# Performance work log

Measured on AMD Instinct MI355X. Metric: run time of the kernel, lower is better.

## Reference

```python
import jax, jax.numpy as jnp
import numpy as np

EMB_DIM = 768
NUM_HEADS = 12
OUT_DIM = 768


def setup_inputs() -> dict:
    key = jax.random.key(0)
    k_x, k_q, k_k, k_v, k_o = jax.random.split(key, 5)
    B, N, D = 8, 1024, EMB_DIM
    s = 1.0 / np.sqrt(D)
    return {
        "x": jax.random.normal(k_x, (B, N, D), dtype=jnp.float32),
        # torch nn.Linear weights are stored [out_features, in_features]
        "Wq": jax.random.normal(k_q, (D, D), dtype=jnp.float32) * s,
        "Wk": jax.random.normal(k_k, (D, D), dtype=jnp.float32) * s,
        "Wv": jax.random.normal(k_v, (D, D), dtype=jnp.float32) * s,
        "Wo": jax.random.normal(k_o, (OUT_DIM, D), dtype=jnp.float32) * s,
    }


def _split_heads(t, H):
    # [B, N, D] -> [B*H, N, D//H]  (heads folded into batch, per einsum 'b i d')
    B, N, D = t.shape
    return t.reshape(B, N, H, D // H).transpose(0, 2, 1, 3).reshape(B * H, N, D // H)


def _merge_heads(t, B, H):
    BH, N, dh = t.shape
    return t.reshape(B, H, N, dh).transpose(0, 2, 1, 3).reshape(B, N, H * dh)


def reference(x, Wq, Wk, Wv, Wo):
    B, N, D = x.shape
    H = NUM_HEADS
    dh = D // H
    # q/k/v projections (torch Linear: y = x @ W.T, no bias)
    q = _split_heads(x @ Wq.T, H)
    k = _split_heads(x @ Wk.T, H)
    v = _split_heads(x @ Wv.T, H)
    scale = dh ** (-0.5)
    # dots: 'b i d , b j d -> b i j' -> full [B*H, N, N] score matrix
    dots = jnp.einsum('bid,bjd->bij', q, k) * scale
    attn = jax.nn.softmax(dots, axis=-1)
    # dropout p=0.0 -> identity
    # vect: 'b i d , b d j -> b i j' == attn @ v
    vect = jnp.einsum('bij,bjd->bid', attn, v)
    out = _merge_heads(vect, B, H) @ Wo.T
    return out
```

## Files before the change

### kernel.cpp

```cpp
#include <hip/hip_runtime.h>
#include <hip/hip_bf16.h>
#include <stdint.h>


typedef __bf16 bf16x8 __attribute__((ext_vector_type(8)));
typedef __bf16 bf16x4 __attribute__((ext_vector_type(4)));
typedef float f32x4 __attribute__((ext_vector_type(4)));

#define GAS __attribute__((address_space(1)))
#define LAS __attribute__((address_space(3)))

__device__ __forceinline__ void glds16(const short* gp, short* lp) {
  __builtin_amdgcn_global_load_lds((const GAS void*)gp, (LAS void*)lp, 16, 0, 0);
}

__device__ __forceinline__ float fast_exp2(float x) {
#if __has_builtin(__builtin_amdgcn_exp2f)
  return __builtin_amdgcn_exp2f(x);
#else
  return __expf(x * 0.6931471805599453f);
#endif
}

__device__ __forceinline__ short bfbits(float f) {
  __bf16 b = (__bf16)f;
  union { __bf16 b; short s; } cv; cv.b = b;
  return cv.s;
}

__device__ __forceinline__ void stage8_f32(const float* __restrict__ src, short* dst) {
  float4 f0 = ((const float4*)src)[0];
  float4 f1 = ((const float4*)src)[1];
  bf16x8 t;
  t[0] = (__bf16)f0.x; t[1] = (__bf16)f0.y; t[2] = (__bf16)f0.z; t[3] = (__bf16)f0.w;
  t[4] = (__bf16)f1.x; t[5] = (__bf16)f1.y; t[6] = (__bf16)f1.z; t[7] = (__bf16)f1.w;
  *(bf16x8*)dst = t;
}

__global__ __launch_bounds__(256) void convert_kernel(
    const float* __restrict__ x, const float* __restrict__ Wq,
    const float* __restrict__ Wk, const float* __restrict__ Wv,
    const float* __restrict__ Wo,
    short* __restrict__ xb, short* __restrict__ wqkv, short* __restrict__ wob) {
  int u0 = blockIdx.x * 1024 + threadIdx.x;
#pragma unroll
  for (int i = 0; i < 4; ++i) {
    int u = u0 + i * 256;
    const float* src; short* dst;
    if (u < 786432) { src = x + (size_t)u * 8; dst = xb + (size_t)u * 8; }
    else if (u < 1007616) {
      int r = u - 786432;
      int wsel = r / 73728, off = r % 73728;
      const float* W = (wsel == 0) ? Wq : (wsel == 1) ? Wk : Wv;
      src = W + (size_t)off * 8;
      dst = wqkv + (size_t)r * 8;
    } else {
      int r = u - 1007616;
      src = Wo + (size_t)r * 8; dst = wob + (size_t)r * 8;
    }
    stage8_f32(src, dst);
  }
}

__device__ __forceinline__ void stage_half(const short* __restrict__ g, short* l,
                                           int w, int lane) {
#pragma unroll
  for (int p = 0; p < 2; ++p) {
    int c = (w * 2 + p) * 64 + lane;
    int row = c >> 3;
    int cs = ((c & 7) ^ (row & 7)) * 8;
    glds16(g + (size_t)row * 768 + cs, l + c * 8);
  }
}

__device__ __forceinline__ void bar_fence() {
  asm volatile("" ::: "memory");
  __builtin_amdgcn_s_barrier();
  asm volatile("" ::: "memory");
}

__device__ __forceinline__ void load_a8(const short* base, int wr, int l16, int quad,
                                        bf16x8 (&fa)[4][2]) {
#pragma unroll
  for (int mf = 0; mf < 4; ++mf)
#pragma unroll
    for (int kk = 0; kk < 2; ++kk) {
      int row = wr * 64 + mf * 16 + l16;
      fa[mf][kk] = *(const bf16x8*)&base[row * 64 + ((((kk << 2) + quad) ^ (row & 7)) << 3)];
    }
}

__device__ __forceinline__ void load_b4(const short* base, int rbase, int l16, int quad,
                                        bf16x8 (&fb)[2][2]) {
#pragma unroll
  for (int nf = 0; nf < 2; ++nf)
#pragma unroll
    for (int kk = 0; kk < 2; ++kk) {
      int row = rbase + nf * 16 + l16;
      fb[nf][kk] = *(const bf16x8*)&base[row * 64 + ((((kk << 2) + quad) ^ (row & 7)) << 3)];
    }
}

__device__ __forceinline__ void mma16(const bf16x8 (&fa)[4][2], const bf16x8 (&fb)[2][2],
                                      f32x4 (&acc)[4][4], int nf0) {
  __builtin_amdgcn_s_setprio(1);
#pragma unroll
  for (int kk = 0; kk < 2; ++kk)
#pragma unroll
    for (int mf = 0; mf < 4; ++mf)
#pragma unroll
      for (int nf = 0; nf < 2; ++nf)
        acc[mf][nf0 + nf] = __builtin_amdgcn_mfma_f32_16x16x32_bf16(
            fa[mf][kk], fb[nf][kk], acc[mf][nf0 + nf], 0, 0, 0);
  __builtin_amdgcn_s_setprio(0);
}

__global__ __launch_bounds__(512, 2) void gemm_qkv(
    const short* __restrict__ xb, const short* __restrict__ wqkv,
    short* __restrict__ q, short* __restrict__ k, short* __restrict__ vt) {
  const int lin = blockIdx.x;
  const int xcd = lin & 7, grp = lin >> 3;
  const int by = grp >> 3;
  const int bx = xcd * 8 + (grp & 7);
  const int m0 = bx * 128;
  const int n0g = by * 256;
  const int tid = threadIdx.x;
  const int w = tid >> 6, lane = tid & 63, l16 = lane & 15, quad = lane >> 4;
  const int wr = w >> 2, wc = w & 3;

  __shared__ short lds[3][24576];

  const short* Asrc = xb + (size_t)m0 * 768;
  const short* Bsrc = wqkv + (size_t)n0g * 768;

  f32x4 acc[4][4];
#pragma unroll
  for (int i = 0; i < 4; ++i)
#pragma unroll
    for (int j = 0; j < 4; ++j) acc[i][j] = (f32x4){0.f, 0.f, 0.f, 0.f};

  stage_half(Asrc, &lds[0][0], w, lane);
  stage_half(Bsrc, &lds[0][8192], w, lane);
  stage_half(Bsrc + 98304, &lds[0][16384], w, lane);
  stage_half(Asrc + 64, &lds[1][0], w, lane);
  stage_half(Bsrc + 64, &lds[1][8192], w, lane);
  stage_half(Bsrc + 98304 + 64, &lds[1][16384], w, lane);
  asm volatile("s_waitcnt vmcnt(6)" ::: "memory");
  bar_fence();

  const int bh = wc >> 1;
  const int rb0 = (wc & 1) * 64;

  bf16x8 fa[4][2], fb0[2][2], fb1[2][2];

#pragma unroll
  for (int t = 0; t < 12; ++t) {
    const int buf = t % 3, nb = (t + 2) % 3;
    const bool pf = (t < 10);
    const short* A = &lds[buf][0];
    const short* Bb = &lds[buf][8192 + bh * 8192];

    load_a8(A, wr, l16, quad, fa);
    load_b4(Bb, rb0, l16, quad, fb0);
    if (pf) {
      stage_half(Asrc + (size_t)(t + 2) * 64, &lds[nb][0], w, lane);
      stage_half(Bsrc + (size_t)(t + 2) * 64, &lds[nb][8192], w, lane);
    }
    bar_fence();
    __builtin_amdgcn_sched_barrier(0);
    mma16(fa, fb0, acc, 0);
    __builtin_amdgcn_sched_barrier(0);
    bar_fence();

    load_b4(Bb, rb0 + 32, l16, quad, fb1);
    if (pf) {
      stage_half(Bsrc + 98304 + (size_t)(t + 2) * 64, &lds[nb][16384], w, lane);
      asm volatile("s_waitcnt vmcnt(6)" ::: "memory");
    } else if (t == 10) {
      asm volatile("s_waitcnt vmcnt(0)" ::: "memory");
    }
    bar_fence();
    __builtin_amdgcn_sched_barrier(0);
    mma16(fa, fb1, acc, 2);
    __builtin_amdgcn_sched_barrier(0);
    bar_fence();
  }

  const int wsel = by / 3;
  const int nl0 = (by % 3) * 256 + wc * 64;
  if (wsel == 2) {
#pragma unroll
    for (int mf = 0; mf < 4; ++mf)
#pragma unroll
      for (int nf = 0; nf < 4; ++nf) {
        int token = m0 + wr * 64 + mf * 16 + quad * 4;
        int nl = nl0 + nf * 16 + l16;
        int bhh = (token >> 10) * 12 + (nl >> 6);
        short tmp[4];
#pragma unroll
        for (int r = 0; r < 4; ++r) tmp[r] = bfbits(acc[mf][nf][r]);
        *(uint2*)(vt + (size_t)bhh * 65536 + (size_t)(nl & 63) * 1024 + (token & 1023)) =
            *(const uint2*)tmp;
      }
  } else {
    short* C = wsel ? k : q;
    const float sc = wsel ? 1.0f : 0.1803368801111244f;
#pragma unroll
    for (int mf = 0; mf < 4; ++mf)
#pragma unroll
      for (int nf = 0; nf < 4; ++nf)
#pragma unroll
        for (int r = 0; r < 4; ++r) {
          int row = m0 + wr * 64 + mf * 16 + quad * 4 + r;
          int nl = nl0 + nf * 16 + l16;
          C[(size_t)row * 768 + nl] = bfbits(acc[mf][nf][r] * sc);
        }
  }
}

__global__ __launch_bounds__(256, 3) void attn_kernel(
    const short* __restrict__ q, const short* __restrict__ k,
    const short* __restrict__ vt, short* __restrict__ vect) {
  const int bh = blockIdx.x % 96;
  const int qt = blockIdx.x / 96;
  const int b = bh / 12, h = bh % 12;
  const int m0 = qt * 128;
  const int tid = threadIdx.x;
  const int w = tid >> 6, lane = tid & 63, l16 = lane & 15, quad = lane >> 4;

  __shared__ short sK[128 * 64];
  __shared__ short sVt[64 * 128];

  const size_t base = (size_t)b * 786432 + (size_t)h * 64;
  const size_t vbase = (size_t)bh * 65536;

#pragma unroll
  for (int p = 0; p < 4; ++p) {
    int lin = (w * 4 + p) * 64 + lane;
    int row = lin >> 3;
    int cs = ((lin & 7) ^ (row & 7)) * 8;
    glds16(q + base + (size_t)(m0 + row) * 768 + cs, &sK[lin * 8]);
  }
  __syncthreads();
  bf16x8 bq[2][2];
#pragma unroll
  for (int g = 0; g < 2; ++g)
#pragma unroll
    for (int kk = 0; kk < 2; ++kk) {
      int row = g * 64 + w * 16 + l16;
      bq[g][kk] = *(const bf16x8*)&sK[row * 64 + (((kk * 4 + quad) ^ (row & 7)) << 3)];
    }

  f32x4 l4[2];
  l4[0] = (f32x4){0.f, 0.f, 0.f, 0.f};
  l4[1] = (f32x4){0.f, 0.f, 0.f, 0.f};
  f32x4 oacc[2][4];
#pragma unroll
  for (int g = 0; g < 2; ++g)
#pragma unroll
    for (int td = 0; td < 4; ++td) oacc[g][td] = (f32x4){0.f, 0.f, 0.f, 0.f};

  for (int j0 = 0; j0 < 1024; j0 += 128) {
    __syncthreads();
#pragma unroll
    for (int p = 0; p < 4; ++p) {
      int lin = (w * 4 + p) * 64 + lane;
      int row = lin >> 3;
      int cs = ((lin & 7) ^ (row & 7)) * 8;
      glds16(k + base + (size_t)(j0 + row) * 768 + cs, &sK[lin * 8]);
    }
#pragma unroll
    for (int p = 0; p < 4; ++p) {
      int lin = (w * 4 + p) * 64 + lane;
      int row = lin >> 4;
      int c = lin & 15;
      int cs = (c ^ (row & 15)) * 8;
      glds16(vt + vbase + (size_t)row * 1024 + j0 + cs, &sVt[lin * 8]);
    }
    __syncthreads();

#pragma unroll
    for (int jh = 0; jh < 2; ++jh) {
      f32x4 s[2][4];
#pragma unroll
      for (int g = 0; g < 2; ++g)
#pragma unroll
        for (int ti = 0; ti < 4; ++ti) s[g][ti] = (f32x4){0.f, 0.f, 0.f, 0.f};
#pragma unroll
      for (int kk = 0; kk < 2; ++kk)
#pragma unroll
        for (int ti = 0; ti < 4; ++ti) {
          int row = jh * 64 + ti * 16 + l16;
          bf16x8 a = *(const bf16x8*)&sK[row * 64 + (((kk * 4 + quad) ^ (row & 7)) << 3)];
          s[0][ti] = __builtin_amdgcn_mfma_f32_16x16x32_bf16(a, bq[0][kk], s[0][ti], 0, 0, 0);
          s[1][ti] = __builtin_amdgcn_mfma_f32_16x16x32_bf16(a, bq[1][kk], s[1][ti], 0, 0, 0);
        }

      bf16x4 pb[2][4];
#pragma unroll
      for (int g = 0; g < 2; ++g)
#pragma unroll
        for (int ti = 0; ti < 4; ++ti) {
          f32x4 e;
          e[0] = fast_exp2(s[g][ti][0]);
          e[1] = fast_exp2(s[g][ti][1]);
          e[2] = fast_exp2(s[g][ti][2]);
          e[3] = fast_exp2(s[g][ti][3]);
          l4[g] += e;
          bf16x4 tb;
          tb[0] = (__bf16)e[0]; tb[1] = (__bf16)e[1];
          tb[2] = (__bf16)e[2]; tb[3] = (__bf16)e[3];
          pb[g][ti] = tb;
        }

#pragma unroll
      for (int t2 = 0; t2 < 2; ++t2) {
        union { bf16x4 hh[2]; bf16x8 v; } bp0, bp1;
        bp0.hh[0] = pb[0][2 * t2];
        bp0.hh[1] = pb[0][2 * t2 + 1];
        bp1.hh[0] = pb[1][2 * t2];
        bp1.hh[1] = pb[1][2 * t2 + 1];
#pragma unroll
        for (int td = 0; td < 4; ++td) {
          int row = td * 16 + l16;
          int o1 = jh * 64 + t2 * 32 + quad * 4;
          int c1 = o1 >> 3, w1 = o1 & 7;
          int c2 = c1 + 2;
          union { uint2 u[2]; bf16x8 v; } tmp;
          tmp.u[0] = *(const uint2*)&sVt[row * 128 + ((c1 ^ (row & 15)) << 3) + w1];
          tmp.u[1] = *(const uint2*)&sVt[row * 128 + ((c2 ^ (row & 15)) << 3) + w1];
          oacc[0][td] = __builtin_amdgcn_mfma_f32_16x16x32_bf16(tmp.v, bp0.v, oacc[0][td], 0, 0, 0);
          oacc[1][td] = __builtin_amdgcn_mfma_f32_16x16x32_bf16(tmp.v, bp1.v, oacc[1][td], 0, 0, 0);
        }
      }
    }
  }

#pragma unroll
  for (int g = 0; g < 2; ++g) {
    float l = (l4[g][0] + l4[g][1]) + (l4[g][2] + l4[g][3]);
    l += __shfl_xor(l, 16);
    l += __shfl_xor(l, 32);
    float inv = 1.0f / l;
    int i_tok = m0 + g * 64 + w * 16 + l16;
#pragma unroll
    for (int td = 0; td < 4; ++td) {
      short tmp[4];
#pragma unroll
      for (int r = 0; r < 4; ++r) tmp[r] = bfbits(oacc[g][td][r] * inv);
      *(uint2*)(vect + base + (size_t)i_tok * 768 + td * 16 + quad * 4) = *(const uint2*)tmp;
    }
  }
}

__global__ __launch_bounds__(256) void gemm_out(
    const short* __restrict__ vect, const short* __restrict__ wob,
    float* __restrict__ out) {
  const int m0 = blockIdx.x * 64;
  const int n0 = blockIdx.y * 128;
  const int tid = threadIdx.x;
  const int w = tid >> 6, lane = tid & 63, l16 = lane & 15, quad = lane >> 4;
  const int wr = w >> 1, wc = w & 1;

  __shared__ short sA[64 * 64];
  __shared__ short sB[128 * 64];

  f32x4 acc[2][4];
#pragma unroll
  for (int i = 0; i < 2; ++i)
#pragma unroll
    for (int j = 0; j < 4; ++j) acc[i][j] = (f32x4){0.f, 0.f, 0.f, 0.f};

  for (int k0 = 0; k0 < 768; k0 += 64) {
    __syncthreads();
    const short* Ab = vect + (size_t)m0 * 768 + k0;
    const short* Bb = wob + (size_t)n0 * 768 + k0;
#pragma unroll
    for (int p = 0; p < 2; ++p) {
      int lin = (w * 2 + p) * 64 + lane;
      int row = lin >> 3;
      int cs = ((lin & 7) ^ (row & 7)) * 8;
      glds16(Ab + (size_t)row * 768 + cs, &sA[lin * 8]);
    }
#pragma unroll
    for (int p = 0; p < 4; ++p) {
      int lin = (w * 4 + p) * 64 + lane;
      int row = lin >> 3;
      int cs = ((lin & 7) ^ (row & 7)) * 8;
      glds16(Bb + (size_t)row * 768 + cs, &sB[lin * 8]);
    }
    __syncthreads();
#pragma unroll
    for (int kk2 = 0; kk2 < 2; ++kk2) {
      bf16x8 af[2], bfg[4];
#pragma unroll
      for (int t = 0; t < 2; ++t) {
        int ra = wr * 32 + t * 16 + l16;
        af[t] = *(const bf16x8*)&sA[ra * 64 + (((kk2 * 4 + quad) ^ (ra & 7)) << 3)];
      }
#pragma unroll
      for (int t = 0; t < 4; ++t) {
        int rb = wc * 64 + t * 16 + l16;
        bfg[t] = *(const bf16x8*)&sB[rb * 64 + (((kk2 * 4 + quad) ^ (rb & 7)) << 3)];
      }
#pragma unroll
      for (int ti = 0; ti < 2; ++ti)
#pragma unroll
        for (int tj = 0; tj < 4; ++tj)
          acc[ti][tj] = __builtin_amdgcn_mfma_f32_16x16x32_bf16(af[ti], bfg[tj], acc[ti][tj], 0, 0, 0);
    }
  }
#pragma unroll
  for (int ti = 0; ti < 2; ++ti)
#pragma unroll
    for (int tj = 0; tj < 4; ++tj)
#pragma unroll
      for (int r = 0; r < 4; ++r) {
        int row = m0 + wr * 32 + ti * 16 + quad * 4 + r;
        int col = n0 + wc * 64 + tj * 16 + l16;
        out[(size_t)row * 768 + col] = acc[ti][tj][r];
      }
}

extern "C" void kernel_launch(void* const* d_in, const int* in_sizes, int n_in,
                              void* d_out, int out_size, void* d_ws, size_t ws_size,
                              hipStream_t stream) {
  const float* x  = (const float*)d_in[0];
  const float* Wq = (const float*)d_in[1];
  const float* Wk = (const float*)d_in[2];
  const float* Wv = (const float*)d_in[3];
  const float* Wo = (const float*)d_in[4];
  float* out = (float*)d_out;

  const size_t MN = (size_t)8192 * 768;
  short* q    = (short*)d_ws;
  short* k    = q + MN;
  short* vt   = k + MN;
  short* vect = q;
  short* wob  = vt + MN;

  short* xb   = (short*)d_out;
  short* wqkv = xb + MN;

  convert_kernel<<<1056, 256, 0, stream>>>(x, Wq, Wk, Wv, Wo, xb, wqkv, wob);
  gemm_qkv<<<576, 512, 0, stream>>>(xb, wqkv, q, k, vt);
  attn_kernel<<<768, 256, 0, stream>>>(q, k, vt, vect);
  gemm_out<<<dim3(128, 6), 256, 0, stream>>>(vect, wob, out);
}
```

Baseline: 182.6 us.

## Software-pipeline attention K/V loads and rewrite output GEMM with triple-buffered tiles

The attention loop now issues the next K tile while the softmax P·V phase runs, and the next V tile after P·V, using explicit vmcnt waits and raw barriers instead of two full syncthreads per iteration. The output projection GEMM is rebuilt as a 512-thread 128x192 tile kernel with a three-stage LDS ring, XCD-aware block mapping and split MFMA phases, matching the QKV GEMM design. Both changes aim to hide global-load latency and cut barrier stalls. In exchange they depend on hand-counted waitcnt values and use more LDS and registers per block.

```diff
diff --git a/kernel.cpp b/kernel.cpp
--- a/kernel.cpp
+++ b/kernel.cpp
@@ -73,6 +73,17 @@
   }
 }
 
+__device__ __forceinline__ void stage_b192(const short* __restrict__ g, short* l,
+                                           int w, int lane) {
+#pragma unroll
+  for (int p = 0; p < 3; ++p) {
+    int c = (w * 3 + p) * 64 + lane;
+    int row = c >> 3;
+    int cs = ((c & 7) ^ (row & 7)) * 8;
+    glds16(g + (size_t)row * 768 + cs, l + c * 8);
+  }
+}
+
 __device__ __forceinline__ void bar_fence() {
   asm volatile("" ::: "memory");
   __builtin_amdgcn_s_barrier();
@@ -101,6 +112,15 @@
     }
 }
 
+__device__ __forceinline__ void load_b2(const short* base, int rbase, int l16, int quad,
+                                        bf16x8 (&fb)[2]) {
+#pragma unroll
+  for (int kk = 0; kk < 2; ++kk) {
+    int row = rbase + l16;
+    fb[kk] = *(const bf16x8*)&base[row * 64 + ((((kk << 2) + quad) ^ (row & 7)) << 3)];
+  }
+}
+
 __device__ __forceinline__ void mma16(const bf16x8 (&fa)[4][2], const bf16x8 (&fb)[2][2],
                                       f32x4 (&acc)[4][4], int nf0) {
   __builtin_amdgcn_s_setprio(1);
@@ -112,6 +132,32 @@
       for (int nf = 0; nf < 2; ++nf)
         acc[mf][nf0 + nf] = __builtin_amdgcn_mfma_f32_16x16x32_bf16(
             fa[mf][kk], fb[nf][kk], acc[mf][nf0 + nf], 0, 0, 0);
+  __builtin_amdgcn_s_setprio(0);
+}
+
+__device__ __forceinline__ void mma16o(const bf16x8 (&fa)[4][2], const bf16x8 (&fb)[2][2],
+                                       f32x4 (&acc)[4][3]) {
+  __builtin_amdgcn_s_setprio(1);
+#pragma unroll
+  for (int kk = 0; kk < 2; ++kk)
+#pragma unroll
+    for (int mf = 0; mf < 4; ++mf)
+#pragma unroll
+      for (int nf = 0; nf < 2; ++nf)
+        acc[mf][nf] = __builtin_amdgcn_mfma_f32_16x16x32_bf16(
+            fa[mf][kk], fb[nf][kk], acc[mf][nf], 0, 0, 0);
+  __builtin_amdgcn_s_setprio(0);
+}
+
+__device__ __forceinline__ void mma8o(const bf16x8 (&fa)[4][2], const bf16x8 (&fb)[2],
+                                      f32x4 (&acc)[4][3]) {
+  __builtin_amdgcn_s_setprio(1);
+#pragma unroll
+  for (int kk = 0; kk < 2; ++kk)
+#pragma unroll
+    for (int mf = 0; mf < 4; ++mf)
+      acc[mf][2] = __builtin_amdgcn_mfma_f32_16x16x32_bf16(
+          fa[mf][kk], fb[kk], acc[mf][2], 0, 0, 0);
   __builtin_amdgcn_s_setprio(0);
 }
 
@@ -218,6 +264,29 @@
   }
 }
 
+__device__ __forceinline__ void attn_stage_k(const short* __restrict__ kb, int j0,
+                                             short* sK, int w, int lane) {
+#pragma unroll
+  for (int p = 0; p < 4; ++p) {
+    int lin = (w * 4 + p) * 64 + lane;
+    int row = lin >> 3;
+    int cs = ((lin & 7) ^ (row & 7)) * 8;
+    glds16(kb + (size_t)(j0 + row) * 768 + cs, &sK[lin * 8]);
+  }
+}
+
+__device__ __forceinline__ void attn_stage_v(const short* __restrict__ vb, int j0,
+                                             short* sVt, int w, int lane) {
+#pragma unroll
+  for (int p = 0; p < 4; ++p) {
+    int lin = (w * 4 + p) * 64 + lane;
+    int row = lin >> 4;
+    int c = lin & 15;
+    int cs = (c ^ (row & 15)) * 8;
+    glds16(vb + (size_t)row * 1024 + j0 + cs, &sVt[lin * 8]);
+  }
+}
+
 __global__ __launch_bounds__(256, 3) void attn_kernel(
     const short* __restrict__ q, const short* __restrict__ k,
     const short* __restrict__ vt, short* __restrict__ vect) {
@@ -232,7 +301,8 @@
   __shared__ short sVt[64 * 128];
 
   const size_t base = (size_t)b * 786432 + (size_t)h * 64;
-  const size_t vbase = (size_t)bh * 65536;
+  const short* kb = k + base;
+  const short* vb = vt + (size_t)bh * 65536;
 
 #pragma unroll
   for (int p = 0; p < 4; ++p) {
@@ -241,7 +311,8 @@
     int cs = ((lin & 7) ^ (row & 7)) * 8;
     glds16(q + base + (size_t)(m0 + row) * 768 + cs, &sK[lin * 8]);
   }
-  __syncthreads();
+  asm volatile("s_waitcnt vmcnt(0)" ::: "memory");
+  bar_fence();
   bf16x8 bq[2][2];
 #pragma unroll
   for (int g = 0; g < 2; ++g)
@@ -250,6 +321,12 @@
       int row = g * 64 + w * 16 + l16;
       bq[g][kk] = *(const bf16x8*)&sK[row * 64 + (((kk * 4 + quad) ^ (row & 7)) << 3)];
     }
+  asm volatile("s_waitcnt lgkmcnt(0)" ::: "memory");
+  __builtin_amdgcn_sched_barrier(0);
+  bar_fence();
+
+  attn_stage_k(kb, 0, sK, w, lane);
+  attn_stage_v(vb, 0, sVt, w, lane);
 
   f32x4 l4[2];
   l4[0] = (f32x4){0.f, 0.f, 0.f, 0.f};
@@ -260,25 +337,12 @@
 #pragma unroll
     for (int td = 0; td < 4; ++td) oacc[g][td] = (f32x4){0.f, 0.f, 0.f, 0.f};
 
-  for (int j0 = 0; j0 < 1024; j0 += 128) {
-    __syncthreads();
-#pragma unroll
-    for (int p = 0; p < 4; ++p) {
-      int lin = (w * 4 + p) * 64 + lane;
-      int row = lin >> 3;
-      int cs = ((lin & 7) ^ (row & 7)) * 8;
-      glds16(k + base + (size_t)(j0 + row) * 768 + cs, &sK[lin * 8]);
-    }
-#pragma unroll
-    for (int p = 0; p < 4; ++p) {
-      int lin = (w * 4 + p) * 64 + lane;
-      int row = lin >> 4;
-      int c = lin & 15;
-      int cs = (c ^ (row & 15)) * 8;
-      glds16(vt + vbase + (size_t)row * 1024 + j0 + cs, &sVt[lin * 8]);
-    }
-    __syncthreads();
-
+  for (int jt = 0; jt < 8; ++jt) {
+    const int j0 = jt * 128;
+    asm volatile("s_waitcnt vmcnt(4)" ::: "memory");
+    bar_fence();
+
+    bf16x4 pb[2][2][4];
 #pragma unroll
     for (int jh = 0; jh < 2; ++jh) {
       f32x4 s[2][4];
@@ -286,6 +350,7 @@
       for (int g = 0; g < 2; ++g)
 #pragma unroll
         for (int ti = 0; ti < 4; ++ti) s[g][ti] = (f32x4){0.f, 0.f, 0.f, 0.f};
+      __builtin_amdgcn_s_setprio(1);
 #pragma unroll
       for (int kk = 0; kk < 2; ++kk)
 #pragma unroll
@@ -295,8 +360,7 @@
           s[0][ti] = __builtin_amdgcn_mfma_f32_16x16x32_bf16(a, bq[0][kk], s[0][ti], 0, 0, 0);
           s[1][ti] = __builtin_amdgcn_mfma_f32_16x16x32_bf16(a, bq[1][kk], s[1][ti], 0, 0, 0);
         }
-
-      bf16x4 pb[2][4];
+      __builtin_amdgcn_s_setprio(0);
 #pragma unroll
       for (int g = 0; g < 2; ++g)
 #pragma unroll
@@ -310,16 +374,28 @@
           bf16x4 tb;
           tb[0] = (__bf16)e[0]; tb[1] = (__bf16)e[1];
           tb[2] = (__bf16)e[2]; tb[3] = (__bf16)e[3];
-          pb[g][ti] = tb;
+          pb[jh][g][ti] = tb;
         }
-
+    }
+    asm volatile("s_waitcnt lgkmcnt(0)" ::: "memory");
+    __builtin_amdgcn_sched_barrier(0);
+    bar_fence();
+    if (jt < 7) attn_stage_k(kb, j0 + 128, sK, w, lane);
+
+    if (jt < 7) { asm volatile("s_waitcnt vmcnt(4)" ::: "memory"); }
+    else        { asm volatile("s_waitcnt vmcnt(0)" ::: "memory"); }
+    bar_fence();
+
+    __builtin_amdgcn_s_setprio(1);
+#pragma unroll
+    for (int jh = 0; jh < 2; ++jh)
 #pragma unroll
       for (int t2 = 0; t2 < 2; ++t2) {
         union { bf16x4 hh[2]; bf16x8 v; } bp0, bp1;
-        bp0.hh[0] = pb[0][2 * t2];
-        bp0.hh[1] = pb[0][2 * t2 + 1];
-        bp1.hh[0] = pb[1][2 * t2];
-        bp1.hh[1] = pb[1][2 * t2 + 1];
+        bp0.hh[0] = pb[jh][0][2 * t2];
+        bp0.hh[1] = pb[jh][0][2 * t2 + 1];
+        bp1.hh[0] = pb[jh][1][2 * t2];
+        bp1.hh[1] = pb[jh][1][2 * t2 + 1];
 #pragma unroll
         for (int td = 0; td < 4; ++td) {
           int row = td * 16 + l16;
@@ -333,7 +409,11 @@
           oacc[1][td] = __builtin_amdgcn_mfma_f32_16x16x32_bf16(tmp.v, bp1.v, oacc[1][td], 0, 0, 0);
         }
       }
-    }
+    __builtin_amdgcn_s_setprio(0);
+    asm volatile("s_waitcnt lgkmcnt(0)" ::: "memory");
+    __builtin_amdgcn_sched_barrier(0);
+    bar_fence();
+    if (jt < 7) attn_stage_v(vb, j0 + 128, sVt, w, lane);
   }
 
 #pragma unroll
@@ -353,72 +433,79 @@
   }
 }
 
-__global__ __launch_bounds__(256) void gemm_out(
+__global__ __launch_bounds__(512, 2) void gemm_out(
     const short* __restrict__ vect, const short* __restrict__ wob,
     float* __restrict__ out) {
-  const int m0 = blockIdx.x * 64;
-  const int n0 = blockIdx.y * 128;
+  const int lin = blockIdx.x;
+  const int xcd = lin & 7, grp = lin >> 3;
+  const int by = grp >> 3;
+  const int bx = xcd * 8 + (grp & 7);
+  const int m0 = bx * 128;
+  const int n0g = by * 192;
   const int tid = threadIdx.x;
   const int w = tid >> 6, lane = tid & 63, l16 = lane & 15, quad = lane >> 4;
-  const int wr = w >> 1, wc = w & 1;
-
-  __shared__ short sA[64 * 64];
-  __shared__ short sB[128 * 64];
-
-  f32x4 acc[2][4];
-#pragma unroll
-  for (int i = 0; i < 2; ++i)
-#pragma unroll
-    for (int j = 0; j < 4; ++j) acc[i][j] = (f32x4){0.f, 0.f, 0.f, 0.f};
-
-  for (int k0 = 0; k0 < 768; k0 += 64) {
-    __syncthreads();
-    const short* Ab = vect + (size_t)m0 * 768 + k0;
-    const short* Bb = wob + (size_t)n0 * 768 + k0;
-#pragma unroll
-    for (int p = 0; p < 2; ++p) {
-      int lin = (w * 2 + p) * 64 + lane;
-      int row = lin >> 3;
-      int cs = ((lin & 7) ^ (row & 7)) * 8;
-      glds16(Ab + (size_t)row * 768 + cs, &sA[lin * 8]);
-    }
-#pragma unroll
-    for (int p = 0; p < 4; ++p) {
-      int lin = (w * 4 + p) * 64 + lane;
-      int row = lin >> 3;
-      int cs = ((lin & 7) ^ (row & 7)) * 8;
-      glds16(Bb + (size_t)row * 768 + cs, &sB[lin * 8]);
-    }
-    __syncthreads();
-#pragma unroll
-    for (int kk2 = 0; kk2 < 2; ++kk2) {
-      bf16x8 af[2], bfg[4];
-#pragma unroll
-      for (int t = 0; t < 2; ++t) {
-        int ra = wr * 32 + t * 16 + l16;
-        af[t] = *(const bf16x8*)&sA[ra * 64 + (((kk2 * 4 + quad) ^ (ra & 7)) << 3)];
-      }
-#pragma unroll
-      for (int t = 0; t < 4; ++t) {
-        int rb = wc * 64 + t * 16 + l16;
-        bfg[t] = *(const bf16x8*)&sB[rb * 64 + (((kk2 * 4 + quad) ^ (rb & 7)) << 3)];
-      }
-#pragma unroll
-      for (int ti = 0; ti < 2; ++ti)
-#pragma unroll
-        for (int tj = 0; tj < 4; ++tj)
-          acc[ti][tj] = __builtin_amdgcn_mfma_f32_16x16x32_bf16(af[ti], bfg[tj], acc[ti][tj], 0, 0, 0);
-    }
-  }
-#pragma unroll
-  for (int ti = 0; ti < 2; ++ti)
-#pragma unroll
-    for (int tj = 0; tj < 4; ++tj)
+  const int wr = w >> 2, wc = w & 3;
+
+  __shared__ short lds[3][20480];
+
+  const short* Asrc = vect + (size_t)m0 * 768;
+  const short* Bsrc = wob + (size_t)n0g * 768;
+
+  f32x4 acc[4][3];
+#pragma unroll
+  for (int i = 0; i < 4; ++i)
+#pragma unroll
+    for (int j = 0; j < 3; ++j) acc[i][j] = (f32x4){0.f, 0.f, 0.f, 0.f};
+
+  stage_half(Asrc, &lds[0][0], w, lane);
+  stage_b192(Bsrc, &lds[0][8192], w, lane);
+  stage_half(Asrc + 64, &lds[1][0], w, lane);
+  stage_b192(Bsrc + 64, &lds[1][8192], w, lane);
+  asm volatile("s_waitcnt vmcnt(5)" ::: "memory");
+  bar_fence();
+
+  const int rb0 = wc * 48;
+  bf16x8 fa[4][2], fb01[2][2], fb2[2];
+
+#pragma unroll
+  for (int t = 0; t < 12; ++t) {
+    const int buf = t % 3, nb = (t + 2) % 3;
+    const bool pf = (t < 10);
+    const short* A = &lds[buf][0];
+    const short* Bb = &lds[buf][8192];
+
+    load_a8(A, wr, l16, quad, fa);
+    load_b4(Bb, rb0, l16, quad, fb01);
+    if (pf) stage_half(Asrc + (size_t)(t + 2) * 64, &lds[nb][0], w, lane);
+    bar_fence();
+    __builtin_amdgcn_sched_barrier(0);
+    mma16o(fa, fb01, acc);
+    __builtin_amdgcn_sched_barrier(0);
+    bar_fence();
+
+    load_b2(Bb, rb0 + 32, l16, quad, fb2);
+    if (pf) {
+      stage_b192(Bsrc + (size_t)(t + 2) * 64, &lds[nb][8192], w, lane);
+      asm volatile("s_waitcnt vmcnt(5)" ::: "memory");
+    } else if (t == 10) {
+      asm volatile("s_waitcnt vmcnt(0)" ::: "memory");
+    }
+    bar_fence();
+    __builtin_amdgcn_sched_barrier(0);
+    mma8o(fa, fb2, acc);
+    __builtin_amdgcn_sched_barrier(0);
+    bar_fence();
+  }
+
+#pragma unroll
+  for (int mf = 0; mf < 4; ++mf)
+#pragma unroll
+    for (int nf = 0; nf < 3; ++nf)
 #pragma unroll
       for (int r = 0; r < 4; ++r) {
-        int row = m0 + wr * 32 + ti * 16 + quad * 4 + r;
-        int col = n0 + wc * 64 + tj * 16 + l16;
-        out[(size_t)row * 768 + col] = acc[ti][tj][r];
+        int row = m0 + wr * 64 + mf * 16 + quad * 4 + r;
+        int col = n0g + wc * 48 + nf * 16 + l16;
+        out[(size_t)row * 768 + col] = acc[mf][nf][r];
       }
 }
 
@@ -445,5 +532,5 @@
   convert_kernel<<<1056, 256, 0, stream>>>(x, Wq, Wk, Wv, Wo, xb, wqkv, wob);
   gemm_qkv<<<576, 512, 0, stream>>>(xb, wqkv, q, k, vt);
   attn_kernel<<<768, 256, 0, stream>>>(q, k, vt, vect);
-  gemm_out<<<dim3(128, 6), 256, 0, stream>>>(vect, wob, out);
-}
+  gemm_out<<<256, 512, 0, stream>>>(vect, wob, out);
+}
```

Measured after the change: 176.1 us. 3.5% less time.
